# Kernel tuning notes

Measured on AMD Instinct MI355X. Metric: run time of the kernel, lower is better.

## Reference

```python
import jax, jax.numpy as jnp
import numpy as np

INIT_RANGE = 0.02


def setup_inputs() -> dict:
    key = jax.random.key(0)
    ks = jax.random.split(key, 7)
    B, S, E, H, D = 4, 2048, 1024, 16, 64
    return {
        "query": jax.random.normal(ks[0], (B, S, E), dtype=jnp.float32),
        "key": jax.random.normal(ks[1], (B, S, E), dtype=jnp.float32),
        "value": jax.random.normal(ks[2], (B, S, E), dtype=jnp.float32),
        "W_Q": jax.random.normal(ks[3], (H, E, D), dtype=jnp.float32) * INIT_RANGE,
        "W_K": jax.random.normal(ks[4], (H, E, D), dtype=jnp.float32) * INIT_RANGE,
        "W_V": jax.random.normal(ks[5], (H, E, D), dtype=jnp.float32) * INIT_RANGE,
        "W_O": jax.random.normal(ks[6], (H, D, E), dtype=jnp.float32) * INIT_RANGE,
        "b_Q": jnp.zeros((H, D), dtype=jnp.float32),
        "b_K": jnp.zeros((H, D), dtype=jnp.float32),
        "b_V": jnp.zeros((H, D), dtype=jnp.float32),
        "b_O": jnp.zeros((E,), dtype=jnp.float32),
    }


def reference(query, key, value, W_Q, W_K, W_V, W_O, b_Q, b_K, b_V, b_O):
    head_dim = W_Q.shape[-1]
    scale = 1.0 / jnp.sqrt(jnp.asarray(head_dim, dtype=query.dtype))
    # Per-head projections: [B,S,E] x [H,E,D] -> [B,S,H,D]
    Q = jnp.einsum('bse,hed->bshd', query, W_Q) + b_Q
    K = jnp.einsum('bse,hed->bshd', key, W_K) + b_K
    V = jnp.einsum('bse,hed->bshd', value, W_V) + b_V
    # Scores: [B,H,S_from,S_to]
    scores = jnp.einsum('bfhd,bthd->bhft', Q, K) * scale
    attn = jax.nn.softmax(scores, axis=-1)
    # Weighted values: [B,H,S,D]
    OV = jnp.einsum('bhft,bthd->bhfd', attn, V)
    # Output projection: [B,S,E]
    return jnp.einsum('bhsd,hde->bse', OV, W_O) + b_O
```

## Files before the change

kernel.cpp:

```cpp
#include <hip/hip_runtime.h>
#include <hip/hip_bf16.h>

typedef __attribute__((ext_vector_type(8))) short bf16x8;
typedef __attribute__((ext_vector_type(4))) float f32x4;
typedef __attribute__((ext_vector_type(16))) float f32x16;
typedef __attribute__((ext_vector_type(4))) int i32x4;

#define LOG2E 1.4426950408889634f

__device__ __forceinline__ short f2bf(float f){
  unsigned u = __float_as_uint(f);
  u += 0x7fffu + ((u >> 16) & 1u);
  return (short)(u >> 16);
}
__device__ __forceinline__ unsigned cvtpk(float lo, float hi){
  unsigned r;
  asm("v_cvt_pk_bf16_f32 %0, %1, %2" : "=v"(r) : "v"(lo), "v"(hi));
  return r;
}
__device__ __forceinline__ void plswap(unsigned &a, unsigned &b){
  asm("v_permlane32_swap_b32 %0, %1" : "+v"(a), "+v"(b));
}
__device__ __forceinline__ void gl_lds16(const short* g, short* l){
  __builtin_amdgcn_global_load_lds((const __attribute__((address_space(1))) void*)g,
                                   (__attribute__((address_space(3))) void*)l, 16, 0, 0);
}

__global__ __launch_bounds__(256) void prep_all(const float* __restrict__ xq,
                                                const float* __restrict__ xk,
                                                const float* __restrict__ xv,
                                                short* __restrict__ oq,
                                                short* __restrict__ ok,
                                                short* __restrict__ ov,
                                                const float* __restrict__ Wq,
                                                const float* __restrict__ Wk,
                                                const float* __restrict__ Wv,
                                                short* __restrict__ WqT,
                                                short* __restrict__ WkT,
                                                short* __restrict__ WvT,
                                                const float* __restrict__ Wo,
                                                short* __restrict__ WoT){
  __shared__ short t[64][72];
  int bid = blockIdx.x;
  int tid = threadIdx.x;
  if (bid < 4096){
    int idx = (bid * 256 + tid) * 8;
    #pragma unroll
    for (int a = 0; a < 3; ++a){
      const float* x = a == 0 ? xq : (a == 1 ? xk : xv);
      short* o = a == 0 ? oq : (a == 1 ? ok : ov);
      float4 v0 = *(const float4*)&x[idx];
      float4 v1 = *(const float4*)&x[idx + 4];
      bf16x8 tt;
      tt[0]=f2bf(v0.x); tt[1]=f2bf(v0.y); tt[2]=f2bf(v0.z); tt[3]=f2bf(v0.w);
      tt[4]=f2bf(v1.x); tt[5]=f2bf(v1.y); tt[6]=f2bf(v1.z); tt[7]=f2bf(v1.w);
      *(bf16x8*)&o[idx] = tt;
    }
  } else if (bid < 4352){
    int b2 = bid - 4096;
    int h = b2 >> 4, et = b2 & 15;
    int er = tid >> 2, qc = (tid & 3) * 16;
    #pragma unroll
    for (int a = 0; a < 3; ++a){
      const float* W = a == 0 ? Wq : (a == 1 ? Wk : Wv);
      short* Wt = a == 0 ? WqT : (a == 1 ? WkT : WvT);
      if (a) __syncthreads();
      const float* src = W + h * 65536 + (et * 64 + er) * 64 + qc;
      #pragma unroll
      for (int v = 0; v < 4; ++v){
        float4 f = *(const float4*)(src + v * 4);
        t[qc + v * 4 + 0][er] = f2bf(f.x);
        t[qc + v * 4 + 1][er] = f2bf(f.y);
        t[qc + v * 4 + 2][er] = f2bf(f.z);
        t[qc + v * 4 + 3][er] = f2bf(f.w);
      }
      __syncthreads();
      bf16x8 o0 = *(const bf16x8*)&t[er][qc];
      bf16x8 o1 = *(const bf16x8*)&t[er][qc + 8];
      size_t dst = (size_t)(h * 64 + er) * 1024 + et * 64 + qc;
      *(bf16x8*)&Wt[dst] = o0;
      *(bf16x8*)&Wt[dst + 8] = o1;
    }
  } else {
    int b2 = bid - 4352;
    int bi = b2 >> 4, bj = b2 & 15;
    int r = tid >> 2, qc = (tid & 3) * 16;
    const float* src = Wo + (size_t)(bi * 64 + r) * 1024 + bj * 64 + qc;
    #pragma unroll
    for (int v = 0; v < 4; ++v){
      float4 f = *(const float4*)(src + v * 4);
      t[qc + v * 4 + 0][r] = f2bf(f.x);
      t[qc + v * 4 + 1][r] = f2bf(f.y);
      t[qc + v * 4 + 2][r] = f2bf(f.z);
      t[qc + v * 4 + 3][r] = f2bf(f.w);
    }
    __syncthreads();
    bf16x8 o0 = *(const bf16x8*)&t[r][qc];
    bf16x8 o1 = *(const bf16x8*)&t[r][qc + 8];
    size_t dst = (size_t)(bj * 64 + r) * 1024 + bi * 64 + qc;
    *(bf16x8*)&WoT[dst] = o0;
    *(bf16x8*)&WoT[dst + 8] = o1;
  }
}

__global__ __launch_bounds__(256) void proj3(const short* __restrict__ Xq,
                                             const short* __restrict__ Xk,
                                             const short* __restrict__ Xv,
                                             const short* __restrict__ WqT,
                                             const short* __restrict__ WkT,
                                             const short* __restrict__ WvT,
                                             const float* __restrict__ bq,
                                             const float* __restrict__ bk,
                                             const float* __restrict__ bv,
                                             short* __restrict__ Oq,
                                             short* __restrict__ Ok,
                                             short* __restrict__ Ov){
  __shared__ short Al[128][64];
  __shared__ short Bl[128][64];
  int z = blockIdx.z;
  const short* A    = z == 0 ? Xq : (z == 1 ? Xk : Xv);
  const short* Wt   = z == 0 ? WqT : (z == 1 ? WkT : WvT);
  const float* bias = z == 0 ? bq : (z == 1 ? bk : bv);
  short* Out        = z == 0 ? Oq : (z == 1 ? Ok : Ov);
  float scale = z == 0 ? (LOG2E * 0.125f) : 1.0f;

  int tid = threadIdx.x;
  int bm0 = blockIdx.x * 128, bn0 = blockIdx.y * 128;
  int w = tid >> 6, lane = tid & 63;
  int wm = w >> 1, wn = w & 1;
  int r16 = lane & 15, kblk = lane >> 4;
  int srow = tid >> 3, schunk = tid & 7;

  f32x4 acc[4][4] = {};
  for (int kt = 0; kt < 16; ++kt){
    int k0 = kt * 64;
    __syncthreads();
    #pragma unroll
    for (int p = 0; p < 4; ++p){
      int row = p * 32 + srow;
      int sc = (schunk ^ (row & 7)) * 8;
      gl_lds16(A  + (size_t)(bm0 + row) * 1024 + k0 + sc, &Al[p * 32 + w * 8][0]);
      gl_lds16(Wt + (size_t)(bn0 + row) * 1024 + k0 + sc, &Bl[p * 32 + w * 8][0]);
    }
    __syncthreads();
    bf16x8 af[2][4], bfr[2][4];
    #pragma unroll
    for (int half = 0; half < 2; ++half){
      #pragma unroll
      for (int m = 0; m < 4; ++m){
        int r = wm * 64 + m * 16 + r16;
        af[half][m] = *(bf16x8*)&Al[r][(((half << 2) | kblk) ^ (r & 7)) * 8];
      }
      #pragma unroll
      for (int n = 0; n < 4; ++n){
        int r = wn * 64 + n * 16 + r16;
        bfr[half][n] = *(bf16x8*)&Bl[r][(((half << 2) | kblk) ^ (r & 7)) * 8];
      }
    }
    #pragma unroll
    for (int half = 0; half < 2; ++half)
      #pragma unroll
      for (int m = 0; m < 4; ++m)
        #pragma unroll
        for (int n = 0; n < 4; ++n)
          acc[m][n] = __builtin_amdgcn_mfma_f32_16x16x32_bf16(af[half][m], bfr[half][n], acc[m][n], 0, 0, 0);
  }
  if (z != 2){
    #pragma unroll
    for (int m = 0; m < 4; ++m){
      int grow0 = bm0 + wm * 64 + m * 16 + kblk * 4;
      #pragma unroll
      for (int n = 0; n < 4; ++n){
        int gcol = bn0 + wn * 64 + n * 16 + r16;
        float bv_ = bias[gcol];
        int h = gcol >> 6, d = gcol & 63;
        #pragma unroll
        for (int i = 0; i < 4; ++i){
          int grow = grow0 + i;
          int b = grow >> 11, s = grow & 2047;
          Out[(size_t)((b * 16 + h) * 2048 + s) * 64 + d] = f2bf((acc[m][n][i] + bv_) * scale);
        }
      }
    }
  } else {
    #pragma unroll
    for (int m = 0; m < 4; ++m){
      int grow0 = bm0 + wm * 64 + m * 16 + kblk * 4;
      int b = grow0 >> 11, s = grow0 & 2047;
      #pragma unroll
      for (int n = 0; n < 4; ++n){
        int gcol = bn0 + wn * 64 + n * 16 + r16;
        float bv_ = bias[gcol];
        int h = gcol >> 6, d = gcol & 63;
        short4 o = make_short4(f2bf(acc[m][n][0] + bv_),
                               f2bf(acc[m][n][1] + bv_),
                               f2bf(acc[m][n][2] + bv_),
                               f2bf(acc[m][n][3] + bv_));
        *(short4*)&Out[(size_t)((b * 16 + h) * 64 + d) * 2048 + s] = o;
      }
    }
  }
}

__global__ __launch_bounds__(256) void out_gemm(const short* __restrict__ A,
                                                const short* __restrict__ Wt,
                                                const float* __restrict__ bias,
                                                float* __restrict__ Out){
  __shared__ short Al[128][64];
  __shared__ short Bl[128][64];
  int tid = threadIdx.x;
  int bm0 = blockIdx.x * 128, bn0 = blockIdx.y * 128;
  int w = tid >> 6, lane = tid & 63;
  int wm = w >> 1, wn = w & 1;
  int r16 = lane & 15, kblk = lane >> 4;
  int srow = tid >> 3, schunk = tid & 7;
  f32x4 acc[4][4] = {};
  for (int kt = 0; kt < 16; ++kt){
    int k0 = kt * 64;
    __syncthreads();
    #pragma unroll
    for (int p = 0; p < 4; ++p){
      int row = p * 32 + srow;
      int sc = (schunk ^ (row & 7)) * 8;
      gl_lds16(A  + (size_t)(bm0 + row) * 1024 + k0 + sc, &Al[p * 32 + w * 8][0]);
      gl_lds16(Wt + (size_t)(bn0 + row) * 1024 + k0 + sc, &Bl[p * 32 + w * 8][0]);
    }
    __syncthreads();
    bf16x8 af[2][4], bfr[2][4];
    #pragma unroll
    for (int half = 0; half < 2; ++half){
      #pragma unroll
      for (int m = 0; m < 4; ++m){
        int r = wm * 64 + m * 16 + r16;
        af[half][m] = *(bf16x8*)&Al[r][(((half << 2) | kblk) ^ (r & 7)) * 8];
      }
      #pragma unroll
      for (int n = 0; n < 4; ++n){
        int r = wn * 64 + n * 16 + r16;
        bfr[half][n] = *(bf16x8*)&Bl[r][(((half << 2) | kblk) ^ (r & 7)) * 8];
      }
    }
    #pragma unroll
    for (int half = 0; half < 2; ++half)
      #pragma unroll
      for (int m = 0; m < 4; ++m)
        #pragma unroll
        for (int n = 0; n < 4; ++n)
          acc[m][n] = __builtin_amdgcn_mfma_f32_16x16x32_bf16(af[half][m], bfr[half][n], acc[m][n], 0, 0, 0);
  }
  #pragma unroll
  for (int m = 0; m < 4; ++m){
    int grow0 = bm0 + wm * 64 + m * 16 + kblk * 4;
    #pragma unroll
    for (int n = 0; n < 4; ++n){
      int gcol = bn0 + wn * 64 + n * 16 + r16;
      float bv = bias[gcol];
      #pragma unroll
      for (int i = 0; i < 4; ++i)
        Out[(size_t)(grow0 + i) * 1024 + gcol] = acc[m][n][i] + bv;
    }
  }
}

__device__ __forceinline__ f32x16 mfma32(bf16x8 a, bf16x8 b, f32x16 c){
  return __builtin_amdgcn_mfma_f32_32x32x16_bf16(a, b, c, 0, 0, 0);
}

__device__ __forceinline__ void sm_pack(f32x16& s0, f32x16& s1, float& lrow, bf16x8* pb){
  #pragma unroll
  for (int r = 0; r < 16; ++r) s0[r] = __builtin_amdgcn_exp2f(s0[r]);
  #pragma unroll
  for (int r = 0; r < 16; ++r) s1[r] = __builtin_amdgcn_exp2f(s1[r]);
  float u8_[8];
  #pragma unroll
  for (int r = 0; r < 8; ++r)
    u8_[r] = (s0[r] + s0[r + 8]) + (s1[r] + s1[r + 8]);
  float rs = ((u8_[0] + u8_[1]) + (u8_[2] + u8_[3])) + ((u8_[4] + u8_[5]) + (u8_[6] + u8_[7]));
  lrow += rs;
  #pragma unroll
  for (int cc = 0; cc < 2; ++cc){
    int b0 = cc * 8;
    unsigned u0 = cvtpk(s0[b0 + 0], s0[b0 + 1]);
    unsigned u1 = cvtpk(s0[b0 + 2], s0[b0 + 3]);
    unsigned w0 = cvtpk(s0[b0 + 4], s0[b0 + 5]);
    unsigned w1 = cvtpk(s0[b0 + 6], s0[b0 + 7]);
    plswap(u0, w0); plswap(u1, w1);
    i32x4 pk0; pk0[0] = (int)u0; pk0[1] = (int)u1; pk0[2] = (int)w0; pk0[3] = (int)w1;
    pb[cc] = __builtin_bit_cast(bf16x8, pk0);
    unsigned y0 = cvtpk(s1[b0 + 0], s1[b0 + 1]);
    unsigned y1 = cvtpk(s1[b0 + 2], s1[b0 + 3]);
    unsigned z0 = cvtpk(s1[b0 + 4], s1[b0 + 5]);
    unsigned z1 = cvtpk(s1[b0 + 6], s1[b0 + 7]);
    plswap(y0, z0); plswap(y1, z1);
    i32x4 pk1; pk1[0] = (int)y0; pk1[1] = (int)y1; pk1[2] = (int)z0; pk1[3] = (int)z1;
    pb[2 + cc] = __builtin_bit_cast(bf16x8, pk1);
  }
}

#define ATT_BODY(T, CUR, NXT)                                                          \
  {                                                                                    \
    if ((T) + 1 < 32){                                                                 \
      _Pragma("unroll")                                                                \
      for (int p = 0; p < 2; ++p){                                                     \
        int row = p * 32 + srow;                                                       \
        gl_lds16(Kp + (size_t)(((T) + 1) * 64 + row) * 64 + sx, &Kl[NXT][p * 32 + w * 8][0]); \
        gl_lds16(Vp + (size_t)row * 2048 + ((T) + 1) * 64 + sx, &Vl[NXT][p * 32 + w * 8][0]); \
      }                                                                                \
    }                                                                                  \
    f32x16 sA0 = {}, sA1 = {}, sB0 = {}, sB1 = {};                                     \
    _Pragma("unroll")                                                                  \
    for (int c = 0; c < 4; ++c){                                                       \
      bf16x8 kf0 = *(const bf16x8*)&Kl[CUR][l31][rchunk[c]];                           \
      bf16x8 kf1 = *(const bf16x8*)&Kl[CUR][32 + l31][rchunk[c]];                      \
      sA0 = mfma32(kf0, qfA[c], sA0);                                                  \
      sA1 = mfma32(kf1, qfA[c], sA1);                                                  \
      sB0 = mfma32(kf0, qfB[c], sB0);                                                  \
      sB1 = mfma32(kf1, qfB[c], sB1);                                                  \
    }                                                                                  \
    bf16x8 pbA[4], pbB[4];                                                             \
    sm_pack(sA0, sA1, lrowA, pbA);                                                     \
    sm_pack(sB0, sB1, lrowB, pbB);                                                     \
    _Pragma("unroll")                                                                  \
    for (int c = 0; c < 4; ++c){                                                       \
      bf16x8 vf0 = *(const bf16x8*)&Vl[CUR][l31][rchunk[c]];                           \
      bf16x8 vf1 = *(const bf16x8*)&Vl[CUR][32 + l31][rchunk[c]];                      \
      accA0 = mfma32(vf0, pbA[c], accA0);                                              \
      accA1 = mfma32(vf1, pbA[c], accA1);                                              \
      accB0 = mfma32(vf0, pbB[c], accB0);                                              \
      accB1 = mfma32(vf1, pbB[c], accB1);                                              \
    }                                                                                  \
    __syncthreads();                                                                   \
  }

__global__ __launch_bounds__(256, 2) void attn(const short* __restrict__ Qb,
                                               const short* __restrict__ Kb,
                                               const short* __restrict__ Vtb,
                                               short* __restrict__ OVb){
  __shared__ short Kl[2][64][64];
  __shared__ short Vl[2][64][64];
  int tid = threadIdx.x;
  int w = tid >> 6, lane = tid & 63;
  int l31 = lane & 31, hi = lane >> 5;
  int bh = blockIdx.x & 63, qb = blockIdx.x >> 6;
  const short* Qp = Qb + ((size_t)bh * 2048 + qb * 256 + w * 64) * 64;
  const short* Kp = Kb + (size_t)bh * 2048 * 64;
  const short* Vp = Vtb + (size_t)bh * 64 * 2048;
  int srow = tid >> 3, schunk = tid & 7;
  int sx = (schunk ^ (srow & 7)) * 8;

  int rchunk[4];
  #pragma unroll
  for (int c = 0; c < 4; ++c) rchunk[c] = (((c << 1) | hi) ^ (l31 & 7)) * 8;

  #pragma unroll
  for (int p = 0; p < 2; ++p){
    int row = p * 32 + srow;
    gl_lds16(Kp + (size_t)row * 64 + sx, &Kl[0][p * 32 + w * 8][0]);
    gl_lds16(Vp + (size_t)row * 2048 + sx, &Vl[0][p * 32 + w * 8][0]);
  }

  bf16x8 qfA[4], qfB[4];
  #pragma unroll
  for (int c = 0; c < 4; ++c){
    qfA[c] = *(const bf16x8*)&Qp[l31 * 64 + c * 16 + hi * 8];
    qfB[c] = *(const bf16x8*)&Qp[(32 + l31) * 64 + c * 16 + hi * 8];
  }

  f32x16 accA0 = {}, accA1 = {}, accB0 = {}, accB1 = {};
  float lrowA = 0.f, lrowB = 0.f;
  __syncthreads();

  for (int t = 0; t < 32; t += 2){
    ATT_BODY(t, 0, 1)
    ATT_BODY(t + 1, 1, 0)
  }

  lrowA += __shfl_xor(lrowA, 32);
  lrowB += __shfl_xor(lrowB, 32);

  int b = bh >> 4, h = bh & 15;
  int q0 = qb * 256 + w * 64 + l31;
  float invA = 1.0f / lrowA;
  float invB = 1.0f / lrowB;
  size_t baseA = ((size_t)(b * 2048 + q0)) * 1024 + h * 64;
  size_t baseB = baseA + (size_t)32 * 1024;
  #pragma unroll
  for (int rg = 0; rg < 4; ++rg){
    short4 a0 = make_short4(f2bf(accA0[rg * 4 + 0] * invA), f2bf(accA0[rg * 4 + 1] * invA),
                            f2bf(accA0[rg * 4 + 2] * invA), f2bf(accA0[rg * 4 + 3] * invA));
    *(short4*)&OVb[baseA + rg * 8 + hi * 4] = a0;
    short4 a1 = make_short4(f2bf(accA1[rg * 4 + 0] * invA), f2bf(accA1[rg * 4 + 1] * invA),
                            f2bf(accA1[rg * 4 + 2] * invA), f2bf(accA1[rg * 4 + 3] * invA));
    *(short4*)&OVb[baseA + 32 + rg * 8 + hi * 4] = a1;
    short4 b0 = make_short4(f2bf(accB0[rg * 4 + 0] * invB), f2bf(accB0[rg * 4 + 1] * invB),
                            f2bf(accB0[rg * 4 + 2] * invB), f2bf(accB0[rg * 4 + 3] * invB));
    *(short4*)&OVb[baseB + rg * 8 + hi * 4] = b0;
    short4 b1 = make_short4(f2bf(accB1[rg * 4 + 0] * invB), f2bf(accB1[rg * 4 + 1] * invB),
                            f2bf(accB1[rg * 4 + 2] * invB), f2bf(accB1[rg * 4 + 3] * invB));
    *(short4*)&OVb[baseB + 32 + rg * 8 + hi * 4] = b1;
  }
}

extern "C" void kernel_launch(void* const* d_in, const int* in_sizes, int n_in,
                              void* d_out, int out_size, void* d_ws, size_t ws_size,
                              hipStream_t stream) {
  const float* query = (const float*)d_in[0];
  const float* key_  = (const float*)d_in[1];
  const float* value = (const float*)d_in[2];
  const float* W_Q = (const float*)d_in[3];
  const float* W_K = (const float*)d_in[4];
  const float* W_V = (const float*)d_in[5];
  const float* W_O = (const float*)d_in[6];
  const float* b_Q = (const float*)d_in[7];
  const float* b_K = (const float*)d_in[8];
  const float* b_V = (const float*)d_in[9];
  const float* b_O = (const float*)d_in[10];

  char* ws = (char*)d_ws;
  const size_t MB2 = 2097152, MB16 = 16777216;
  short* WqT = (short*)(ws + 0);
  short* WkT = (short*)(ws + MB2);
  short* WvT = (short*)(ws + 2 * MB2);
  short* WoT = (short*)(ws + 3 * MB2);
  short* Xq = (short*)(ws + 4 * MB2);
  short* Xk = (short*)(ws + 4 * MB2 + MB16);
  short* Xv = (short*)(ws + 4 * MB2 + 2 * MB16);
  bool big = ws_size >= (size_t)(4 * MB2 + 6 * MB16);
  short* Qb  = (short*)(ws + 4 * MB2 + 3 * MB16);
  short* Kb  = big ? (short*)(ws + 4 * MB2 + 4 * MB16) : Xq;
  short* Vtb = big ? (short*)(ws + 4 * MB2 + 5 * MB16) : Xk;
  short* OVb = Xv;

  prep_all<<<4608, 256, 0, stream>>>(query, key_, value, Xq, Xk, Xv,
                                     W_Q, W_K, W_V, WqT, WkT, WvT, W_O, WoT);

  if (big){
    proj3<<<dim3(64, 8, 3), 256, 0, stream>>>(Xq, Xk, Xv, WqT, WkT, WvT,
                                              b_Q, b_K, b_V, Qb, Kb, Vtb);
  } else {
    proj3<<<dim3(64, 8, 1), 256, 0, stream>>>(Xq, Xk, Xv, WqT, WkT, WvT, b_Q, b_K, b_V, Qb, Kb, Vtb);
    proj3<<<dim3(64, 8, 1), 256, 0, stream>>>(Xk, Xk, Xv, WkT, WkT, WvT, b_K, b_K, b_V, Kb, Kb, Vtb);
    proj3<<<dim3(64, 8, 1), 256, 0, stream>>>(Xv, Xk, Xv, WvT, WkT, WvT, b_V, b_K, b_V, Vtb, Kb, Vtb);
  }

  attn<<<512, 256, 0, stream>>>(Qb, Kb, Vtb, OVb);

  out_gemm<<<dim3(64, 8), 256, 0, stream>>>(OVb, WoT, b_O, (float*)d_out);
}
```

Before: 193.7 us.

## Load K/V fragments directly from global memory instead of LDS double buffering

Drops the shared-memory double-buffered staging of K and V tiles, along with the per-tile barrier. Each wave now reads its MFMA operand fragments straight from global memory into registers. This removes LDS traffic and block-wide synchronisation. In exchange, each of the four waves fetches the same K/V data redundantly through the caches, and loads are no longer prefetched a tile ahead, so latency may be exposed.

```diff
diff --git a/kernel.cpp b/kernel.cpp
--- a/kernel.cpp
+++ b/kernel.cpp
@@ -297,67 +297,19 @@
   }
 }
 
-#define ATT_BODY(T, CUR, NXT)                                                          \
-  {                                                                                    \
-    if ((T) + 1 < 32){                                                                 \
-      _Pragma("unroll")                                                                \
-      for (int p = 0; p < 2; ++p){                                                     \
-        int row = p * 32 + srow;                                                       \
-        gl_lds16(Kp + (size_t)(((T) + 1) * 64 + row) * 64 + sx, &Kl[NXT][p * 32 + w * 8][0]); \
-        gl_lds16(Vp + (size_t)row * 2048 + ((T) + 1) * 64 + sx, &Vl[NXT][p * 32 + w * 8][0]); \
-      }                                                                                \
-    }                                                                                  \
-    f32x16 sA0 = {}, sA1 = {}, sB0 = {}, sB1 = {};                                     \
-    _Pragma("unroll")                                                                  \
-    for (int c = 0; c < 4; ++c){                                                       \
-      bf16x8 kf0 = *(const bf16x8*)&Kl[CUR][l31][rchunk[c]];                           \
-      bf16x8 kf1 = *(const bf16x8*)&Kl[CUR][32 + l31][rchunk[c]];                      \
-      sA0 = mfma32(kf0, qfA[c], sA0);                                                  \
-      sA1 = mfma32(kf1, qfA[c], sA1);                                                  \
-      sB0 = mfma32(kf0, qfB[c], sB0);                                                  \
-      sB1 = mfma32(kf1, qfB[c], sB1);                                                  \
-    }                                                                                  \
-    bf16x8 pbA[4], pbB[4];                                                             \
-    sm_pack(sA0, sA1, lrowA, pbA);                                                     \
-    sm_pack(sB0, sB1, lrowB, pbB);                                                     \
-    _Pragma("unroll")                                                                  \
-    for (int c = 0; c < 4; ++c){                                                       \
-      bf16x8 vf0 = *(const bf16x8*)&Vl[CUR][l31][rchunk[c]];                           \
-      bf16x8 vf1 = *(const bf16x8*)&Vl[CUR][32 + l31][rchunk[c]];                      \
-      accA0 = mfma32(vf0, pbA[c], accA0);                                              \
-      accA1 = mfma32(vf1, pbA[c], accA1);                                              \
-      accB0 = mfma32(vf0, pbB[c], accB0);                                              \
-      accB1 = mfma32(vf1, pbB[c], accB1);                                              \
-    }                                                                                  \
-    __syncthreads();                                                                   \
-  }
-
 __global__ __launch_bounds__(256, 2) void attn(const short* __restrict__ Qb,
                                                const short* __restrict__ Kb,
                                                const short* __restrict__ Vtb,
                                                short* __restrict__ OVb){
-  __shared__ short Kl[2][64][64];
-  __shared__ short Vl[2][64][64];
   int tid = threadIdx.x;
   int w = tid >> 6, lane = tid & 63;
   int l31 = lane & 31, hi = lane >> 5;
   int bh = blockIdx.x & 63, qb = blockIdx.x >> 6;
   const short* Qp = Qb + ((size_t)bh * 2048 + qb * 256 + w * 64) * 64;
-  const short* Kp = Kb + (size_t)bh * 2048 * 64;
-  const short* Vp = Vtb + (size_t)bh * 64 * 2048;
-  int srow = tid >> 3, schunk = tid & 7;
-  int sx = (schunk ^ (srow & 7)) * 8;
-
-  int rchunk[4];
-  #pragma unroll
-  for (int c = 0; c < 4; ++c) rchunk[c] = (((c << 1) | hi) ^ (l31 & 7)) * 8;
-
-  #pragma unroll
-  for (int p = 0; p < 2; ++p){
-    int row = p * 32 + srow;
-    gl_lds16(Kp + (size_t)row * 64 + sx, &Kl[0][p * 32 + w * 8][0]);
-    gl_lds16(Vp + (size_t)row * 2048 + sx, &Vl[0][p * 32 + w * 8][0]);
-  }
+  const short* K0 = Kb + (size_t)bh * 2048 * 64 + (size_t)l31 * 64 + hi * 8;
+  const short* K1 = K0 + 32 * 64;
+  const short* V0 = Vtb + (size_t)bh * 64 * 2048 + (size_t)l31 * 2048 + hi * 8;
+  const short* V1 = V0 + (size_t)32 * 2048;
 
   bf16x8 qfA[4], qfB[4];
   #pragma unroll
@@ -368,11 +320,41 @@
 
   f32x16 accA0 = {}, accA1 = {}, accB0 = {}, accB1 = {};
   float lrowA = 0.f, lrowB = 0.f;
-  __syncthreads();
-
-  for (int t = 0; t < 32; t += 2){
-    ATT_BODY(t, 0, 1)
-    ATT_BODY(t + 1, 1, 0)
+
+  for (int t = 0; t < 32; ++t){
+    const short* kt0 = K0 + (size_t)t * 64 * 64;
+    const short* kt1 = K1 + (size_t)t * 64 * 64;
+    const short* vt0 = V0 + t * 64;
+    const short* vt1 = V1 + t * 64;
+    bf16x8 kf0[4], kf1[4], vf0[4], vf1[4];
+    #pragma unroll
+    for (int c = 0; c < 4; ++c){
+      kf0[c] = *(const bf16x8*)(kt0 + c * 16);
+      kf1[c] = *(const bf16x8*)(kt1 + c * 16);
+      vf0[c] = *(const bf16x8*)(vt0 + c * 16);
+      vf1[c] = *(const bf16x8*)(vt1 + c * 16);
+    }
+
+    f32x16 sA0 = {}, sA1 = {}, sB0 = {}, sB1 = {};
+    #pragma unroll
+    for (int c = 0; c < 4; ++c){
+      sA0 = mfma32(kf0[c], qfA[c], sA0);
+      sA1 = mfma32(kf1[c], qfA[c], sA1);
+      sB0 = mfma32(kf0[c], qfB[c], sB0);
+      sB1 = mfma32(kf1[c], qfB[c], sB1);
+    }
+
+    bf16x8 pbA[4], pbB[4];
+    sm_pack(sA0, sA1, lrowA, pbA);
+    sm_pack(sB0, sB1, lrowB, pbB);
+
+    #pragma unroll
+    for (int c = 0; c < 4; ++c){
+      accA0 = mfma32(vf0[c], pbA[c], accA0);
+      accA1 = mfma32(vf1[c], pbA[c], accA1);
+      accB0 = mfma32(vf0[c], pbB[c], accB0);
+      accB1 = mfma32(vf1[c], pbB[c], accB1);
+    }
   }
 
   lrowA += __shfl_xor(lrowA, 32);
```

New measurement: 240.5 us. 1.24x slower.
